# Kernel optimization log

Measured on AMD Instinct MI355X. Metric: run time of the kernel, lower is better.

The kernel has to match this reference:

```python
import jax, jax.numpy as jnp
import numpy as np

H = 8
DK = 32  # head_dim = 256 // 8
SCALE = 1.0 / np.float32(np.sqrt(DK))
EPS = 1e-5


def _ln(x, g, b):
    mu = jnp.mean(x, axis=-1, keepdims=True)
    var = jnp.var(x, axis=-1, keepdims=True)
    return (x - mu) / jnp.sqrt(var + EPS) * g + b


def _lin(x, W, b):
    return x @ W + b


def setup_inputs() -> dict:
    key = jax.random.key(0)
    ks = jax.random.split(key, 16)
    B, M, N, D, F = 4, 64, 512, 256, 1024
    s = 0.02
    inp = {
        "machine_emb": jax.random.normal(ks[0], (B, M, D), jnp.float32),
        "op_emb": jax.random.normal(ks[1], (B, N, D), jnp.float32),
        "edge_emb": jax.random.normal(ks[2], (B, N, M, D), jnp.float32),
        "o2m_mask": jax.random.bernoulli(ks[3], 0.3, (B, N, M)),
    }
    # projection weights stored as (in, out)
    for i, nm in enumerate(["q", "k", "v", "o", "ks", "vs", "e"]):
        inp["W" + nm] = jax.random.normal(ks[4 + i], (D, D), jnp.float32) * s
        inp["b" + nm] = jnp.zeros((D,), jnp.float32)
    # layernorms: norm1 (g1/b1), norm2 (g2/b2), norm_op (gop/bop)
    for nm in ["1", "2", "op"]:
        inp["g" + nm] = jnp.ones((D,), jnp.float32)
        inp["bn" + nm] = jnp.zeros((D,), jnp.float32)
    # FFN
    inp["Wf1"] = jax.random.normal(ks[11], (D, F), jnp.float32) * s
    inp["bf1"] = jnp.zeros((F,), jnp.float32)
    inp["Wf2"] = jax.random.normal(ks[12], (F, D), jnp.float32) * s
    inp["bf2"] = jnp.zeros((D,), jnp.float32)
    return inp


def reference(machine_emb, op_emb, edge_emb, o2m_mask,
              Wq, bq, Wk, bk, Wv, bv, Wo, bo, Wks, bks, Wvs, bvs, We, be,
              g1, bn1, g2, bn2, gop, bnop, Wf1, bf1, Wf2, bf2):
    B, M, D = machine_emb.shape
    N = op_emb.shape[1]

    residual = machine_emb
    machine_norm = _ln(machine_emb, g1, bn1)
    op_norm = _ln(op_emb, gop, bnop)

    # (B, H, M, dk) / (B, H, N, dk)
    q_m = _lin(machine_norm, Wq, bq).reshape(B, M, H, DK).transpose(0, 2, 1, 3)
    k_o = _lin(op_norm, Wk, bk).reshape(B, N, H, DK).transpose(0, 2, 1, 3)
    v_o = _lin(op_norm, Wv, bv).reshape(B, N, H, DK).transpose(0, 2, 1, 3)

    # edge: (B,N,M,D) -> (B,H,M,N,dk)
    edge = _lin(edge_emb, We, be).reshape(B, N, M, H, DK)
    edge = edge.transpose(0, 3, 2, 1, 4)  # bhmnd

    q_total = q_m[:, :, :, None, :] + edge          # (B,H,M,N,dk)
    k_total = k_o[:, :, None, :, :] + edge          # (B,H,M,N,dk)
    v_total = v_o[:, :, None, :, :] + edge          # (B,H,M,N,dk)

    scores = jnp.sum(q_total * k_total, axis=-1) * SCALE  # (B,H,M,N)

    k_self = _lin(machine_norm, Wks, bks).reshape(B, M, H, DK).transpose(0, 2, 1, 3)
    self_scores = jnp.sum(q_m * k_self, axis=-1) * SCALE   # (B,H,M)

    cross_mask = o2m_mask.transpose(0, 2, 1)[:, None, :, :]  # (B,1,M,N)
    combined_scores = jnp.concatenate([self_scores[..., None], scores], axis=-1)  # (B,H,M,1+N)
    self_flag = jnp.ones((B, 1, M, 1), dtype=bool)
    combined_mask = jnp.concatenate([self_flag, jnp.broadcast_to(cross_mask, (B, 1, M, N))], axis=-1)
    combined_scores = jnp.where(combined_mask, combined_scores, -jnp.inf)

    attn = jax.nn.softmax(combined_scores, axis=-1)
    attn = jnp.where(jnp.isnan(attn), 0.0, attn)

    v_self = _lin(machine_norm, Wvs, bvs).reshape(B, M, H, DK).transpose(0, 2, 1, 3)
    combined_values = jnp.concatenate([v_self[:, :, :, None, :], v_total], axis=3)  # (B,H,M,1+N,dk)

    attn_out = jnp.einsum('bhmi,bhmid->bhmd', attn, combined_values)
    attn_out = attn_out.transpose(0, 2, 1, 3).reshape(B, M, D)
    attn_out = _lin(attn_out, Wo, bo)

    machine_emb = residual + attn_out
    h = _ln(machine_emb, g2, bn2)
    ffn = _lin(jax.nn.relu(_lin(h, Wf1, bf1)), Wf2, bf2)
    return machine_emb + ffn
```

## Files before the change

### kernel.cpp

```cpp
#include <hip/hip_runtime.h>
#include <hip/hip_bf16.h>
#include <math.h>

#define H_ 8
#define DK_ 32
#define B_ 4
#define M_ 64
#define N_ 512
#define D_ 256
#define F_ 1024

static constexpr float SCALE = 0.17677669529663687f;
static constexpr float EPS = 1e-5f;

typedef __bf16 bf16x8 __attribute__((ext_vector_type(8)));
typedef float f32x4 __attribute__((ext_vector_type(4)));

__device__ inline float bfbits2f(unsigned int b) {
    union { unsigned int i; float f; } c; c.i = b << 16; return c.f;
}
__device__ inline void unpack8(uint4 u, float* f) {
    f[0] = bfbits2f(u.x & 0xffffu); f[1] = bfbits2f(u.x >> 16);
    f[2] = bfbits2f(u.y & 0xffffu); f[3] = bfbits2f(u.y >> 16);
    f[4] = bfbits2f(u.z & 0xffffu); f[5] = bfbits2f(u.z >> 16);
    f[6] = bfbits2f(u.w & 0xffffu); f[7] = bfbits2f(u.w >> 16);
}

__global__ __launch_bounds__(256) void detect_kernel(const unsigned int* __restrict__ mask,
                                                     int* __restrict__ flags) {
    __shared__ int s2[256];
    int t = threadIdx.x;
    int cgt = 0;
    for (int i = 0; i < 128; ++i) {
        unsigned int w = mask[t * 128 + i];
        if (w > 1u) cgt++;
    }
    s2[t] = cgt;
    __syncthreads();
    if (t == 0) {
        int b = 0;
        for (int i = 0; i < 256; ++i) b += s2[i];
        flags[1] = (b > 0) ? 1 : 0;
    }
}

struct TTArgs {
    const void* src[9];
    void* dst[9];
    int tcum[9];
    int kl[9];
    int nl[9];
};

__global__ __launch_bounds__(256) void prep_transpose(TTArgs a) {
    __shared__ float ld[64][65];
    int bx = blockIdx.x;
    int ti = 0;
    while (bx >= a.tcum[ti]) ti++;
    int j = bx - (ti ? a.tcum[ti - 1] : 0);
    int K = 1 << a.kl[ti], N = 1 << a.nl[ti];
    int ntn = N >> 6;
    int kt = j / ntn, nt = j - kt * ntn;
    const float* src = (const float*)a.src[ti];
    __hip_bfloat16* dst = (__hip_bfloat16*)a.dst[ti];
    int t = threadIdx.x;
    int col = t & 63, r0 = t >> 6;
#pragma unroll
    for (int i = 0; i < 16; ++i) {
        int r = i * 4 + r0;
        ld[r][col] = src[(size_t)(kt * 64 + r) * N + nt * 64 + col];
    }
    __syncthreads();
#pragma unroll
    for (int i = 0; i < 16; ++i) {
        int r = i * 4 + r0;
        dst[(size_t)(nt * 64 + r) * K + kt * 64 + col] = __float2bfloat16(ld[col][r]);
    }
}

__global__ __launch_bounds__(256) void prep_bias(const float* bq, const float* bks,
                                                 const float* bvs, const float* bk,
                                                 const float* bv,
                                                 float* bqksvs, float* bkv) {
    int t = threadIdx.x;
    bqksvs[t] = bq[t];
    bqksvs[256 + t] = bks[t];
    bqksvs[512 + t] = bvs[t];
    bkv[t] = bk[t];
    bkv[256 + t] = bv[t];
}

__device__ inline float block_reduce256(float v, bool is_max, float* sbuf) {
#pragma unroll
    for (int off = 32; off > 0; off >>= 1) {
        float o = __shfl_down(v, off, 64);
        v = is_max ? fmaxf(v, o) : (v + o);
    }
    int lane = threadIdx.x & 63, wid = threadIdx.x >> 6;
    if (lane == 0) sbuf[wid] = v;
    __syncthreads();
    float r;
    if (is_max) r = fmaxf(fmaxf(sbuf[0], sbuf[1]), fmaxf(sbuf[2], sbuf[3]));
    else        r = sbuf[0] + sbuf[1] + sbuf[2] + sbuf[3];
    __syncthreads();
    return r;
}

__global__ __launch_bounds__(256) void ln_kernel(const float* __restrict__ xin,
                                                 const float* __restrict__ g,
                                                 const float* __restrict__ bta,
                                                 __hip_bfloat16* __restrict__ out) {
    __shared__ float sbuf[4];
    int row = blockIdx.x, d = threadIdx.x;
    size_t idx = (size_t)row * 256 + d;
    float x = xin[idx];
    float s  = block_reduce256(x, false, sbuf);
    float ss = block_reduce256(x * x, false, sbuf);
    float mu = s * (1.f / 256.f);
    float var = ss * (1.f / 256.f) - mu * mu;
    float y = (x - mu) * rsqrtf(var + EPS) * g[d] + bta[d];
    out[idx] = __float2bfloat16(y);
}

__global__ __launch_bounds__(256) void gemm64(const __hip_bfloat16* __restrict__ A,
                                              const __hip_bfloat16* __restrict__ BT,
                                              const float* __restrict__ bias,
                                              const float* __restrict__ resid,
                                              void* __restrict__ out,
                                              int K, int ldc, int flags) {
    __shared__ __align__(16) __bf16 As[64 * 40];
    __shared__ __align__(16) __bf16 Bs[64 * 40];
    const int rowBase = blockIdx.x * 64;
    const int colBase = blockIdx.y * 64;
    const int t = threadIdx.x;
    const int w = t >> 6;
    const int l = t & 63;
    const int lrow = l & 15;
    const int lk8 = (l >> 4) * 8;
    const int ar = t >> 2;
    const int ac = (t & 3) * 8;

    f32x4 acc[4] = {};
    for (int k0 = 0; k0 < K; k0 += 32) {
        bf16x8 av = *(const bf16x8*)(A + (size_t)(rowBase + ar) * K + k0 + ac);
        bf16x8 bv = *(const bf16x8*)(BT + (size_t)(colBase + ar) * K + k0 + ac);
        __syncthreads();
        *(bf16x8*)(As + ar * 40 + ac) = av;
        *(bf16x8*)(Bs + ar * 40 + ac) = bv;
        __syncthreads();
        bf16x8 af = *(const bf16x8*)(As + (w * 16 + lrow) * 40 + lk8);
#pragma unroll
        for (int c = 0; c < 4; ++c) {
            bf16x8 bf = *(const bf16x8*)(Bs + (c * 16 + lrow) * 40 + lk8);
            acc[c] = __builtin_amdgcn_mfma_f32_16x16x32_bf16(af, bf, acc[c], 0, 0, 0);
        }
    }
    int rbase = rowBase + w * 16 + ((l >> 4) * 4);
#pragma unroll
    for (int c = 0; c < 4; ++c) {
        int col = colBase + c * 16 + (l & 15);
        float bb = bias[col];
#pragma unroll
        for (int r = 0; r < 4; ++r) {
            int row = rbase + r;
            size_t oi = (size_t)row * ldc + col;
            float v = acc[c][r] + bb;
            if (flags & 1) v = fmaxf(v, 0.f);
            if (flags & 4) v += resid[oi];
            if (flags & 8) ((float*)out)[oi] = v;
            else ((__hip_bfloat16*)out)[oi] = __float2bfloat16(v);
        }
    }
}

__global__ __launch_bounds__(256) void edge_gemm4(const float* __restrict__ E,
                                                  const __hip_bfloat16* __restrict__ WeT,
                                                  const float* __restrict__ be,
                                                  const __hip_bfloat16* __restrict__ qkvs,
                                                  const __hip_bfloat16* __restrict__ kov,
                                                  const void* __restrict__ mask,
                                                  const int* __restrict__ flags,
                                                  __hip_bfloat16* __restrict__ eperm,
                                                  float* __restrict__ scBn) {
    __shared__ __align__(16) __bf16 smem[64 * 272];
    __bf16* As = smem;
    __bf16* Cs = smem;
    const int bn = blockIdx.x;
    const int b = bn >> 9, n = bn & 511;
    const int t = threadIdx.x;
    const int w = t >> 6;
    const int l = t & 63;
    const int lrow = l & 15;
    const int lk8 = (l >> 4) * 8;
    const int ar = t >> 2;
    const int ac = (t & 3) * 8;
    const float* Ab = E + (size_t)bn * 64 * 256;

    f32x4 acc[4][4] = {};
    for (int k0 = 0; k0 < 256; k0 += 32) {
        const float* ap = Ab + (size_t)ar * 256 + k0 + ac;
        float4 x0 = *(const float4*)ap;
        float4 x1 = *(const float4*)(ap + 4);
        bf16x8 av;
        av[0] = (__bf16)x0.x; av[1] = (__bf16)x0.y; av[2] = (__bf16)x0.z; av[3] = (__bf16)x0.w;
        av[4] = (__bf16)x1.x; av[5] = (__bf16)x1.y; av[6] = (__bf16)x1.z; av[7] = (__bf16)x1.w;
        __syncthreads();
        *(bf16x8*)(As + ar * 40 + ac) = av;
        __syncthreads();
        bf16x8 af[4];
#pragma unroll
        for (int rr = 0; rr < 4; ++rr)
            af[rr] = *(const bf16x8*)(As + (rr * 16 + lrow) * 40 + lk8);
#pragma unroll
        for (int c = 0; c < 4; ++c) {
            bf16x8 bf = *(const bf16x8*)(WeT + (size_t)(w * 64 + c * 16 + lrow) * 256 + k0 + lk8);
#pragma unroll
            for (int rr = 0; rr < 4; ++rr)
                acc[rr][c] = __builtin_amdgcn_mfma_f32_16x16x32_bf16(af[rr], bf, acc[rr][c], 0, 0, 0);
        }
    }
    __syncthreads();
#pragma unroll
    for (int c = 0; c < 4; ++c) {
        int col = w * 64 + c * 16 + (l & 15);
        float bb = be[col];
#pragma unroll
        for (int rr = 0; rr < 4; ++rr) {
#pragma unroll
            for (int r = 0; r < 4; ++r) {
                int m = rr * 16 + (l >> 4) * 4 + r;
                Cs[m * 272 + col] = (__bf16)(acc[rr][c][r] + bb);
            }
        }
    }
    __syncthreads();
    const bool u8 = flags[1] != 0;
    const int seg = t & 31;
    const int h = seg >> 2;
    const int dk8 = (seg & 3) * 8;
#pragma unroll
    for (int j = 0; j < 8; ++j) {
        int m = j * 8 + (t >> 5);
        uint4 ev4 = *(const uint4*)(Cs + m * 272 + seg * 8);
        size_t bhm = (size_t)((b * 8 + h) * 64 + m);
        *(uint4*)(eperm + (bhm * 512 + n) * 32 + dk8) = ev4;
        float ev[8], qf[8], kf[8];
        unpack8(ev4, ev);
        uint4 qv4 = *(const uint4*)(qkvs + (size_t)(b * 64 + m) * 768 + h * 32 + dk8);
        uint4 kv4 = *(const uint4*)(kov + (size_t)(b * 512 + n) * 512 + h * 32 + dk8);
        unpack8(qv4, qf);
        unpack8(kv4, kf);
        float p = 0.f;
#pragma unroll
        for (int i = 0; i < 8; ++i)
            p += (qf[i] + ev[i]) * (kf[i] + ev[i]);
        p += __shfl_xor(p, 1, 64);
        p += __shfl_xor(p, 2, 64);
        if ((t & 3) == 0) {
            int mi = (b * 512 + n) * 64 + m;
            int mk = u8 ? (int)((const unsigned char*)mask)[mi] : ((const int*)mask)[mi];
            scBn[(size_t)bn * 512 + h * 64 + m] = mk ? p * SCALE : -__builtin_inff();
        }
    }
}

__global__ __launch_bounds__(256) void transpose_sc(const float* __restrict__ in,
                                                    float* __restrict__ out) {
    __shared__ float ld[64][65];
    int b = blockIdx.z;
    int n0 = blockIdx.x * 64;
    int hm0 = blockIdx.y * 64;
    int t = threadIdx.x;
    int col = t & 63, r0 = t >> 6;
#pragma unroll
    for (int i = 0; i < 16; ++i) {
        int r = i * 4 + r0;
        ld[r][col] = in[((size_t)(b * 512 + n0 + r)) * 512 + hm0 + col];
    }
    __syncthreads();
#pragma unroll
    for (int i = 0; i < 16; ++i) {
        int r = i * 4 + r0;
        out[((size_t)(b * 512 + hm0 + r)) * 512 + n0 + col] = ld[col][r];
    }
}

__global__ __launch_bounds__(256) void smax_attnout(const float* __restrict__ sc,
                                                    const __hip_bfloat16* __restrict__ qkvs,
                                                    const __hip_bfloat16* __restrict__ kov,
                                                    const __hip_bfloat16* __restrict__ eperm,
                                                    __hip_bfloat16* __restrict__ AO) {
    __shared__ float sbuf[4];
    __shared__ float attnS[512];
    __shared__ float selfSc;
    __shared__ float selfA;
    __shared__ float red[16][8];
    int bhm = blockIdx.x;
    int m = bhm & 63;
    int h = (bhm >> 6) & 7;
    int b = bhm >> 9;
    int t = threadIdx.x;
    if (t == 0) {
        const __hip_bfloat16* q  = qkvs + (size_t)(b * 64 + m) * 768 + h * 32;
        const __hip_bfloat16* ks = q + 256;
        float s = 0.f;
        for (int i = 0; i < 32; ++i) s += __bfloat162float(q[i]) * __bfloat162float(ks[i]);
        selfSc = s * SCALE;
    }
    __syncthreads();
    float sv = selfSc;
    float s0 = sc[(size_t)bhm * 512 + t];
    float s1 = sc[(size_t)bhm * 512 + 256 + t];
    float mx = block_reduce256(fmaxf(fmaxf(s0, s1), sv), true, sbuf);
    float e0 = __expf(s0 - mx);
    float e1 = __expf(s1 - mx);
    float eself = __expf(sv - mx);
    float sum = block_reduce256(e0 + e1 + (t == 0 ? eself : 0.f), false, sbuf);
    float inv = 1.f / sum;
    attnS[t] = e0 * inv;
    attnS[256 + t] = e1 * inv;
    if (t == 0) selfA = eself * inv;
    __syncthreads();

    const int d8 = (t & 3) * 8;
    const int ng = t >> 2;
    const int w = t >> 6, l = t & 63;
    const __hip_bfloat16* ebase = eperm + (size_t)bhm * 512 * 32;
    const __hip_bfloat16* vbase = kov + (size_t)(b * 512) * 512 + 256 + h * 32;
    float accv[8] = {};
#pragma unroll
    for (int i = 0; i < 8; ++i) {
        int n = ng + i * 64;
        float a = attnS[n];
        float ev[8], vv[8];
        uint4 e4 = *(const uint4*)(ebase + (size_t)n * 32 + d8);
        uint4 v4 = *(const uint4*)(vbase + (size_t)n * 512 + d8);
        unpack8(e4, ev);
        unpack8(v4, vv);
#pragma unroll
        for (int k = 0; k < 8; ++k) accv[k] += a * (vv[k] + ev[k]);
    }
#pragma unroll
    for (int off = 4; off <= 32; off <<= 1) {
#pragma unroll
        for (int k = 0; k < 8; ++k) accv[k] += __shfl_xor(accv[k], off, 64);
    }
    if ((l >> 2) == 0) {
#pragma unroll
        for (int k = 0; k < 8; ++k) red[w * 4 + (l & 3)][k] = accv[k];
    }
    __syncthreads();
    if (t < 32) {
        int slot = t >> 3, elem = t & 7;
        float r = red[slot][elem] + red[4 + slot][elem] + red[8 + slot][elem] + red[12 + slot][elem];
        float vs = __bfloat162float(qkvs[(size_t)(b * 64 + m) * 768 + 512 + h * 32 + t]);
        r += selfA * vs;
        AO[(size_t)(b * 64 + m) * 256 + h * 32 + t] = __float2bfloat16(r);
    }
}

extern "C" void kernel_launch(void* const* d_in, const int* in_sizes, int n_in,
                              void* d_out, int out_size, void* d_ws, size_t ws_size,
                              hipStream_t stream) {
    const float* machine_emb = (const float*)d_in[0];
    const float* op_emb      = (const float*)d_in[1];
    const float* edge_emb    = (const float*)d_in[2];
    const void*  o2m_mask    = d_in[3];

    char* p = (char*)d_ws;
    int* flags = (int*)p;                        p += 256;
    __hip_bfloat16* WqksvsT = (__hip_bfloat16*)p; p += 196608 * 2;
    __hip_bfloat16* WkvT    = (__hip_bfloat16*)p; p += 131072 * 2;
    __hip_bfloat16* WoT     = (__hip_bfloat16*)p; p += 65536 * 2;
    __hip_bfloat16* WeT     = (__hip_bfloat16*)p; p += 65536 * 2;
    __hip_bfloat16* Wf1T    = (__hip_bfloat16*)p; p += 262144 * 2;
    __hip_bfloat16* Wf2T    = (__hip_bfloat16*)p; p += 262144 * 2;
    float* bqksvs           = (float*)p;          p += 768 * 4;
    float* bkv              = (float*)p;          p += 512 * 4;
    __hip_bfloat16* mnorm   = (__hip_bfloat16*)p; p += 65536 * 2;
    __hip_bfloat16* onorm   = (__hip_bfloat16*)p; p += 524288 * 2;
    __hip_bfloat16* qkvs    = (__hip_bfloat16*)p; p += 196608 * 2;
    __hip_bfloat16* kov     = (__hip_bfloat16*)p; p += 1048576 * 2;
    __hip_bfloat16* eperm   = (__hip_bfloat16*)p; p += (size_t)33554432 * 2;
    float* scBn      = (float*)p;                p += (size_t)1048576 * 4;
    float* scT       = (float*)p;                p += (size_t)1048576 * 4;
    __hip_bfloat16* AO = (__hip_bfloat16*)p;     p += 65536 * 2;
    float* m2        = (float*)p;                p += 65536 * 4;
    __hip_bfloat16* hn = (__hip_bfloat16*)p;     p += 65536 * 2;
    __hip_bfloat16* h1 = (__hip_bfloat16*)p;     p += 262144 * 2;

    TTArgs ta;
    const int srcIdx[9] = {4, 12, 14, 6, 8, 10, 16, 24, 26};
    void* dsts[9] = {WqksvsT, WqksvsT + 65536, WqksvsT + 131072,
                     WkvT, WkvT + 65536, WoT, WeT, Wf1T, Wf2T};
    const int kl9[9] = {8, 8, 8, 8, 8, 8, 8, 8, 10};
    const int nl9[9] = {8, 8, 8, 8, 8, 8, 8, 10, 8};
    int tcum = 0;
    for (int i = 0; i < 9; ++i) {
        ta.src[i] = d_in[srcIdx[i]];
        ta.dst[i] = dsts[i];
        int tiles = (1 << (kl9[i] - 6)) * (1 << (nl9[i] - 6));
        tcum += tiles;
        ta.tcum[i] = tcum;
        ta.kl[i] = kl9[i];
        ta.nl[i] = nl9[i];
    }

    hipLaunchKernelGGL(detect_kernel, dim3(1), dim3(256), 0, stream,
                       (const unsigned int*)o2m_mask, flags);
    hipLaunchKernelGGL(prep_transpose, dim3(tcum), dim3(256), 0, stream, ta);
    hipLaunchKernelGGL(prep_bias, dim3(1), dim3(256), 0, stream,
                       (const float*)d_in[5], (const float*)d_in[13],
                       (const float*)d_in[15], (const float*)d_in[7],
                       (const float*)d_in[9], bqksvs, bkv);

    hipLaunchKernelGGL(ln_kernel, dim3(256), dim3(256), 0, stream,
                       machine_emb, (const float*)d_in[18], (const float*)d_in[19], mnorm);
    hipLaunchKernelGGL(ln_kernel, dim3(2048), dim3(256), 0, stream,
                       op_emb, (const float*)d_in[22], (const float*)d_in[23], onorm);

    hipLaunchKernelGGL(gemm64, dim3(4, 12), dim3(256), 0, stream,
                       mnorm, WqksvsT, bqksvs, nullptr, qkvs, 256, 768, 0);
    hipLaunchKernelGGL(gemm64, dim3(32, 8), dim3(256), 0, stream,
                       onorm, WkvT, bkv, nullptr, kov, 256, 512, 0);

    hipLaunchKernelGGL(edge_gemm4, dim3(2048), dim3(256), 0, stream,
                       edge_emb, WeT, (const float*)d_in[17],
                       qkvs, kov, o2m_mask, flags, eperm, scBn);

    hipLaunchKernelGGL(transpose_sc, dim3(8, 8, 4), dim3(256), 0, stream, scBn, scT);

    hipLaunchKernelGGL(smax_attnout, dim3(2048), dim3(256), 0, stream,
                       scT, qkvs, kov, eperm, AO);

    hipLaunchKernelGGL(gemm64, dim3(4, 4), dim3(256), 0, stream,
                       AO, WoT, (const float*)d_in[11], machine_emb, m2, 256, 256, 4 | 8);
    hipLaunchKernelGGL(ln_kernel, dim3(256), dim3(256), 0, stream,
                       m2, (const float*)d_in[20], (const float*)d_in[21], hn);
    hipLaunchKernelGGL(gemm64, dim3(4, 16), dim3(256), 0, stream,
                       hn, Wf1T, (const float*)d_in[25], nullptr, h1, 256, 1024, 1);
    hipLaunchKernelGGL(gemm64, dim3(4, 4), dim3(256), 0, stream,
                       h1, Wf2T, (const float*)d_in[27], m2, (float*)d_out, 1024, 256, 4 | 8);
}
```

Before: 379.4 us.

## Fuse edge projection, scores, softmax and PV into flash-style kernel with split merge

Replaces the edge GEMM, score transpose and softmax/attention-output kernels with a single flash-attention-style kernel. Each block owns one (b, m) and a quarter of the ops, computes the edge projection with MFMA and applies an online softmax. A small merge kernel then combines the four partial results with the self-attention term. This removes the large materialised bf16 edge tensor (eperm) and the score round-trips through global memory. In exchange the edge reads become strided across n (64*256 floats apart), the k/v loads are scalar, and there are fewer blocks (1024 instead of 2048).

```diff
diff --git a/kernel.cpp b/kernel.cpp
--- a/kernel.cpp
+++ b/kernel.cpp
@@ -18,12 +18,6 @@
 
 __device__ inline float bfbits2f(unsigned int b) {
     union { unsigned int i; float f; } c; c.i = b << 16; return c.f;
-}
-__device__ inline void unpack8(uint4 u, float* f) {
-    f[0] = bfbits2f(u.x & 0xffffu); f[1] = bfbits2f(u.x >> 16);
-    f[2] = bfbits2f(u.y & 0xffffu); f[3] = bfbits2f(u.y >> 16);
-    f[4] = bfbits2f(u.z & 0xffffu); f[5] = bfbits2f(u.z >> 16);
-    f[6] = bfbits2f(u.w & 0xffffu); f[7] = bfbits2f(u.w >> 16);
 }
 
 __global__ __launch_bounds__(256) void detect_kernel(const unsigned int* __restrict__ mask,
@@ -173,190 +167,220 @@
     }
 }
 
-__global__ __launch_bounds__(256) void edge_gemm4(const float* __restrict__ E,
+__global__ __launch_bounds__(256) void edge_flash(const float* __restrict__ E,
                                                   const __hip_bfloat16* __restrict__ WeT,
                                                   const float* __restrict__ be,
                                                   const __hip_bfloat16* __restrict__ qkvs,
                                                   const __hip_bfloat16* __restrict__ kov,
                                                   const void* __restrict__ mask,
                                                   const int* __restrict__ flags,
-                                                  __hip_bfloat16* __restrict__ eperm,
-                                                  float* __restrict__ scBn) {
-    __shared__ __align__(16) __bf16 smem[64 * 272];
-    __bf16* As = smem;
-    __bf16* Cs = smem;
-    const int bn = blockIdx.x;
-    const int b = bn >> 9, n = bn & 511;
+                                                  float* __restrict__ fPV,
+                                                  float* __restrict__ fML) {
+    __shared__ float mbias[128];
+    const int bid = blockIdx.x;
+    const int b  = bid >> 8;
+    const int qq = (bid >> 6) & 3;
+    const int m  = bid & 63;
+    const int n0 = qq * 128;
     const int t = threadIdx.x;
     const int w = t >> 6;
     const int l = t & 63;
-    const int lrow = l & 15;
-    const int lk8 = (l >> 4) * 8;
-    const int ar = t >> 2;
-    const int ac = (t & 3) * 8;
-    const float* Ab = E + (size_t)bn * 64 * 256;
-
-    f32x4 acc[4][4] = {};
-    for (int k0 = 0; k0 < 256; k0 += 32) {
-        const float* ap = Ab + (size_t)ar * 256 + k0 + ac;
-        float4 x0 = *(const float4*)ap;
-        float4 x1 = *(const float4*)(ap + 4);
-        bf16x8 av;
-        av[0] = (__bf16)x0.x; av[1] = (__bf16)x0.y; av[2] = (__bf16)x0.z; av[3] = (__bf16)x0.w;
-        av[4] = (__bf16)x1.x; av[5] = (__bf16)x1.y; av[6] = (__bf16)x1.z; av[7] = (__bf16)x1.w;
-        __syncthreads();
-        *(bf16x8*)(As + ar * 40 + ac) = av;
-        __syncthreads();
-        bf16x8 af[4];
-#pragma unroll
-        for (int rr = 0; rr < 4; ++rr)
-            af[rr] = *(const bf16x8*)(As + (rr * 16 + lrow) * 40 + lk8);
-#pragma unroll
-        for (int c = 0; c < 4; ++c) {
-            bf16x8 bf = *(const bf16x8*)(WeT + (size_t)(w * 64 + c * 16 + lrow) * 256 + k0 + lk8);
+    const int l15 = l & 15;
+    const int lh  = l >> 4;
+
+    if (t < 128) {
+        int n = n0 + t;
+        int mi = (b * 512 + n) * 64 + m;
+        int mk = (flags[1] != 0) ? (int)((const unsigned char*)mask)[mi]
+                                 : ((const int*)mask)[mi];
+        mbias[t] = mk ? 0.f : -1e30f;
+    }
+
+    int   col[4];
+    float qv[4], bev[4];
+#pragma unroll
+    for (int c = 0; c < 4; ++c) {
+        col[c] = w * 64 + c * 16 + l15;
+        qv[c]  = __bfloat162float(qkvs[(size_t)(b * 64 + m) * 768 + col[c]]);
+        bev[c] = be[col[c]];
+    }
+    const __hip_bfloat16* kvb = kov + (size_t)b * 512 * 512;
+    __syncthreads();
+
+    float M[2] = {-1e25f, -1e25f};
+    float L[2] = {0.f, 0.f};
+    float PV[2][2] = {{0.f, 0.f}, {0.f, 0.f}};
+
+    for (int nt = 0; nt < 2; ++nt) {
+        const int ns = n0 + nt * 64;
+        f32x4 acc[4][4] = {};
+        const float* apb = E + ((size_t)((b * 512 + ns + l15) * 64 + m)) * 256 + lh * 8;
+#pragma unroll 2
+        for (int k0 = 0; k0 < 256; k0 += 32) {
+            bf16x8 af[4];
+#pragma unroll
+            for (int rr = 0; rr < 4; ++rr) {
+                const float* ap = apb + (size_t)rr * (16 * 64 * 256) + k0;
+                float4 x0 = *(const float4*)ap;
+                float4 x1 = *(const float4*)(ap + 4);
+                bf16x8 v;
+                v[0] = (__bf16)x0.x; v[1] = (__bf16)x0.y; v[2] = (__bf16)x0.z; v[3] = (__bf16)x0.w;
+                v[4] = (__bf16)x1.x; v[5] = (__bf16)x1.y; v[6] = (__bf16)x1.z; v[7] = (__bf16)x1.w;
+                af[rr] = v;
+            }
+#pragma unroll
+            for (int c = 0; c < 4; ++c) {
+                bf16x8 bv = *(const bf16x8*)(WeT + (size_t)col[c] * 256 + k0 + lh * 8);
+#pragma unroll
+                for (int rr = 0; rr < 4; ++rr)
+                    acc[rr][c] = __builtin_amdgcn_mfma_f32_16x16x32_bf16(af[rr], bv, acc[rr][c], 0, 0, 0);
+            }
+        }
+
+        float s[4][2][4];
+#pragma unroll
+        for (int rr = 0; rr < 4; ++rr) {
+            const int nb = ns + rr * 16 + lh * 4;
+#pragma unroll
+            for (int r = 0; r < 4; ++r) {
+                const size_t krow = (size_t)(nb + r) * 512;
+                float p0 = 0.f, p1 = 0.f;
+#pragma unroll
+                for (int ce = 0; ce < 2; ++ce) {
+                    {
+                        const int c = ce;
+                        float kf = __bfloat162float(kvb[krow + col[c]]);
+                        float ef = acc[rr][c][r] + bev[c];
+                        p0 += (qv[c] + ef) * (kf + ef);
+                    }
+                    {
+                        const int c = 2 + ce;
+                        float kf = __bfloat162float(kvb[krow + col[c]]);
+                        float ef = acc[rr][c][r] + bev[c];
+                        p1 += (qv[c] + ef) * (kf + ef);
+                    }
+                }
+                s[rr][0][r] = p0;
+                s[rr][1][r] = p1;
+            }
+        }
+#pragma unroll
+        for (int rr = 0; rr < 4; ++rr) {
+#pragma unroll
+            for (int r = 0; r < 4; ++r) {
+                float mb = mbias[nt * 64 + rr * 16 + lh * 4 + r];
+#pragma unroll
+                for (int hp = 0; hp < 2; ++hp) {
+                    float v = s[rr][hp][r];
+                    v += __shfl_xor(v, 1);
+                    v += __shfl_xor(v, 2);
+                    v += __shfl_xor(v, 4);
+                    v += __shfl_xor(v, 8);
+                    s[rr][hp][r] = v * SCALE + mb;
+                }
+            }
+        }
+#pragma unroll
+        for (int hp = 0; hp < 2; ++hp) {
+            float tm = s[0][hp][0];
 #pragma unroll
             for (int rr = 0; rr < 4; ++rr)
-                acc[rr][c] = __builtin_amdgcn_mfma_f32_16x16x32_bf16(af[rr], bf, acc[rr][c], 0, 0, 0);
-        }
-    }
-    __syncthreads();
-#pragma unroll
-    for (int c = 0; c < 4; ++c) {
-        int col = w * 64 + c * 16 + (l & 15);
-        float bb = be[col];
+#pragma unroll
+                for (int r = 0; r < 4; ++r) tm = fmaxf(tm, s[rr][hp][r]);
+            tm = fmaxf(tm, __shfl_xor(tm, 16));
+            tm = fmaxf(tm, __shfl_xor(tm, 32));
+            float Mn = fmaxf(M[hp], tm);
+            float f = __expf(M[hp] - Mn);
+            M[hp] = Mn;
+            L[hp] *= f;
+            PV[hp][0] *= f;
+            PV[hp][1] *= f;
+        }
 #pragma unroll
         for (int rr = 0; rr < 4; ++rr) {
-#pragma unroll
-            for (int r = 0; r < 4; ++r) {
-                int m = rr * 16 + (l >> 4) * 4 + r;
-                Cs[m * 272 + col] = (__bf16)(acc[rr][c][r] + bb);
-            }
-        }
-    }
-    __syncthreads();
-    const bool u8 = flags[1] != 0;
-    const int seg = t & 31;
-    const int h = seg >> 2;
-    const int dk8 = (seg & 3) * 8;
-#pragma unroll
-    for (int j = 0; j < 8; ++j) {
-        int m = j * 8 + (t >> 5);
-        uint4 ev4 = *(const uint4*)(Cs + m * 272 + seg * 8);
-        size_t bhm = (size_t)((b * 8 + h) * 64 + m);
-        *(uint4*)(eperm + (bhm * 512 + n) * 32 + dk8) = ev4;
-        float ev[8], qf[8], kf[8];
-        unpack8(ev4, ev);
-        uint4 qv4 = *(const uint4*)(qkvs + (size_t)(b * 64 + m) * 768 + h * 32 + dk8);
-        uint4 kv4 = *(const uint4*)(kov + (size_t)(b * 512 + n) * 512 + h * 32 + dk8);
-        unpack8(qv4, qf);
-        unpack8(kv4, kf);
-        float p = 0.f;
-#pragma unroll
-        for (int i = 0; i < 8; ++i)
-            p += (qf[i] + ev[i]) * (kf[i] + ev[i]);
-        p += __shfl_xor(p, 1, 64);
-        p += __shfl_xor(p, 2, 64);
-        if ((t & 3) == 0) {
-            int mi = (b * 512 + n) * 64 + m;
-            int mk = u8 ? (int)((const unsigned char*)mask)[mi] : ((const int*)mask)[mi];
-            scBn[(size_t)bn * 512 + h * 64 + m] = mk ? p * SCALE : -__builtin_inff();
-        }
-    }
-}
-
-__global__ __launch_bounds__(256) void transpose_sc(const float* __restrict__ in,
-                                                    float* __restrict__ out) {
-    __shared__ float ld[64][65];
-    int b = blockIdx.z;
-    int n0 = blockIdx.x * 64;
-    int hm0 = blockIdx.y * 64;
-    int t = threadIdx.x;
-    int col = t & 63, r0 = t >> 6;
-#pragma unroll
-    for (int i = 0; i < 16; ++i) {
-        int r = i * 4 + r0;
-        ld[r][col] = in[((size_t)(b * 512 + n0 + r)) * 512 + hm0 + col];
-    }
-    __syncthreads();
-#pragma unroll
-    for (int i = 0; i < 16; ++i) {
-        int r = i * 4 + r0;
-        out[((size_t)(b * 512 + hm0 + r)) * 512 + n0 + col] = ld[col][r];
-    }
-}
-
-__global__ __launch_bounds__(256) void smax_attnout(const float* __restrict__ sc,
-                                                    const __hip_bfloat16* __restrict__ qkvs,
-                                                    const __hip_bfloat16* __restrict__ kov,
-                                                    const __hip_bfloat16* __restrict__ eperm,
-                                                    __hip_bfloat16* __restrict__ AO) {
-    __shared__ float sbuf[4];
-    __shared__ float attnS[512];
-    __shared__ float selfSc;
-    __shared__ float selfA;
-    __shared__ float red[16][8];
-    int bhm = blockIdx.x;
-    int m = bhm & 63;
-    int h = (bhm >> 6) & 7;
-    int b = bhm >> 9;
-    int t = threadIdx.x;
-    if (t == 0) {
-        const __hip_bfloat16* q  = qkvs + (size_t)(b * 64 + m) * 768 + h * 32;
-        const __hip_bfloat16* ks = q + 256;
-        float s = 0.f;
-        for (int i = 0; i < 32; ++i) s += __bfloat162float(q[i]) * __bfloat162float(ks[i]);
-        selfSc = s * SCALE;
-    }
-    __syncthreads();
-    float sv = selfSc;
-    float s0 = sc[(size_t)bhm * 512 + t];
-    float s1 = sc[(size_t)bhm * 512 + 256 + t];
-    float mx = block_reduce256(fmaxf(fmaxf(s0, s1), sv), true, sbuf);
-    float e0 = __expf(s0 - mx);
-    float e1 = __expf(s1 - mx);
-    float eself = __expf(sv - mx);
-    float sum = block_reduce256(e0 + e1 + (t == 0 ? eself : 0.f), false, sbuf);
-    float inv = 1.f / sum;
-    attnS[t] = e0 * inv;
-    attnS[256 + t] = e1 * inv;
-    if (t == 0) selfA = eself * inv;
-    __syncthreads();
-
-    const int d8 = (t & 3) * 8;
-    const int ng = t >> 2;
-    const int w = t >> 6, l = t & 63;
-    const __hip_bfloat16* ebase = eperm + (size_t)bhm * 512 * 32;
-    const __hip_bfloat16* vbase = kov + (size_t)(b * 512) * 512 + 256 + h * 32;
-    float accv[8] = {};
-#pragma unroll
-    for (int i = 0; i < 8; ++i) {
-        int n = ng + i * 64;
-        float a = attnS[n];
-        float ev[8], vv[8];
-        uint4 e4 = *(const uint4*)(ebase + (size_t)n * 32 + d8);
-        uint4 v4 = *(const uint4*)(vbase + (size_t)n * 512 + d8);
-        unpack8(e4, ev);
-        unpack8(v4, vv);
-#pragma unroll
-        for (int k = 0; k < 8; ++k) accv[k] += a * (vv[k] + ev[k]);
-    }
-#pragma unroll
-    for (int off = 4; off <= 32; off <<= 1) {
-#pragma unroll
-        for (int k = 0; k < 8; ++k) accv[k] += __shfl_xor(accv[k], off, 64);
-    }
-    if ((l >> 2) == 0) {
-#pragma unroll
-        for (int k = 0; k < 8; ++k) red[w * 4 + (l & 3)][k] = accv[k];
-    }
-    __syncthreads();
-    if (t < 32) {
-        int slot = t >> 3, elem = t & 7;
-        float r = red[slot][elem] + red[4 + slot][elem] + red[8 + slot][elem] + red[12 + slot][elem];
-        float vs = __bfloat162float(qkvs[(size_t)(b * 64 + m) * 768 + 512 + h * 32 + t]);
-        r += selfA * vs;
-        AO[(size_t)(b * 64 + m) * 256 + h * 32 + t] = __float2bfloat16(r);
-    }
+            const int nb = ns + rr * 16 + lh * 4;
+#pragma unroll
+            for (int hp = 0; hp < 2; ++hp) {
+#pragma unroll
+                for (int r = 0; r < 4; ++r) {
+                    const size_t vrow = (size_t)(nb + r) * 512 + 256;
+                    float a = __expf(s[rr][hp][r] - M[hp]);
+                    L[hp] += a;
+                    float ef0 = acc[rr][2 * hp][r]     + bev[2 * hp];
+                    float ef1 = acc[rr][2 * hp + 1][r] + bev[2 * hp + 1];
+                    float vf0 = __bfloat162float(kvb[vrow + col[2 * hp]]);
+                    float vf1 = __bfloat162float(kvb[vrow + col[2 * hp + 1]]);
+                    PV[hp][0] += a * (ef0 + vf0);
+                    PV[hp][1] += a * (ef1 + vf1);
+                }
+            }
+        }
+    }
+
+#pragma unroll
+    for (int hp = 0; hp < 2; ++hp) {
+        L[hp] += __shfl_xor(L[hp], 16);
+        L[hp] += __shfl_xor(L[hp], 32);
+#pragma unroll
+        for (int ce = 0; ce < 2; ++ce) {
+            PV[hp][ce] += __shfl_xor(PV[hp][ce], 16);
+            PV[hp][ce] += __shfl_xor(PV[hp][ce], 32);
+        }
+    }
+    const int part = (b * 64 + m) * 4 + qq;
+    if (lh == 0) {
+#pragma unroll
+        for (int hp = 0; hp < 2; ++hp) {
+            int h = 2 * w + hp;
+#pragma unroll
+            for (int ce = 0; ce < 2; ++ce)
+                fPV[((size_t)part * 8 + h) * 32 + ce * 16 + l15] = PV[hp][ce];
+            if (l15 == 0) {
+                fML[((size_t)part * 8 + h) * 2 + 0] = M[hp];
+                fML[((size_t)part * 8 + h) * 2 + 1] = L[hp];
+            }
+        }
+    }
+}
+
+__global__ __launch_bounds__(256) void flash_merge(const float* __restrict__ fPV,
+                                                   const float* __restrict__ fML,
+                                                   const __hip_bfloat16* __restrict__ qkvs,
+                                                   __hip_bfloat16* __restrict__ AO) {
+    const int bm = blockIdx.x;
+    const int t = threadIdx.x;
+    const int h = t >> 5, dk = t & 31;
+    const int col = h * 32 + dk;
+    const __hip_bfloat16* qb = qkvs + (size_t)bm * 768;
+    float qf  = __bfloat162float(qb[col]);
+    float ksf = __bfloat162float(qb[256 + col]);
+    float p = qf * ksf;
+    p += __shfl_xor(p, 1);
+    p += __shfl_xor(p, 2);
+    p += __shfl_xor(p, 4);
+    p += __shfl_xor(p, 8);
+    p += __shfl_xor(p, 16);
+    float sself = p * SCALE;
+    float Mst = sself;
+    float Mq[4], Lq[4], Pq[4];
+    const int part0 = bm * 4;
+#pragma unroll
+    for (int q = 0; q < 4; ++q) {
+        Mq[q] = fML[((size_t)(part0 + q) * 8 + h) * 2 + 0];
+        Lq[q] = fML[((size_t)(part0 + q) * 8 + h) * 2 + 1];
+        Pq[q] = fPV[((size_t)(part0 + q) * 8 + h) * 32 + dk];
+        Mst = fmaxf(Mst, Mq[q]);
+    }
+    float fs = __expf(sself - Mst);
+    float Ltot = fs;
+    float Ptot = fs * __bfloat162float(qb[512 + col]);
+#pragma unroll
+    for (int q = 0; q < 4; ++q) {
+        float fq = __expf(Mq[q] - Mst);
+        Ltot += Lq[q] * fq;
+        Ptot += Pq[q] * fq;
+    }
+    AO[(size_t)bm * 256 + col] = __float2bfloat16(Ptot / Ltot);
 }
 
 extern "C" void kernel_launch(void* const* d_in, const int* in_sizes, int n_in,
@@ -381,9 +405,8 @@
     __hip_bfloat16* onorm   = (__hip_bfloat16*)p; p += 524288 * 2;
     __hip_bfloat16* qkvs    = (__hip_bfloat16*)p; p += 196608 * 2;
     __hip_bfloat16* kov     = (__hip_bfloat16*)p; p += 1048576 * 2;
-    __hip_bfloat16* eperm   = (__hip_bfloat16*)p; p += (size_t)33554432 * 2;
-    float* scBn      = (float*)p;                p += (size_t)1048576 * 4;
-    float* scT       = (float*)p;                p += (size_t)1048576 * 4;
+    float* fPV              = (float*)p;          p += 262144 * 4;
+    float* fML              = (float*)p;          p += 16384 * 4;
     __hip_bfloat16* AO = (__hip_bfloat16*)p;     p += 65536 * 2;
     float* m2        = (float*)p;                p += 65536 * 4;
     __hip_bfloat16* hn = (__hip_bfloat16*)p;     p += 65536 * 2;
@@ -424,14 +447,12 @@
     hipLaunchKernelGGL(gemm64, dim3(32, 8), dim3(256), 0, stream,
                        onorm, WkvT, bkv, nullptr, kov, 256, 512, 0);
 
-    hipLaunchKernelGGL(edge_gemm4, dim3(2048), dim3(256), 0, stream,
+    hipLaunchKernelGGL(edge_flash, dim3(1024), dim3(256), 0, stream,
                        edge_emb, WeT, (const float*)d_in[17],
-                       qkvs, kov, o2m_mask, flags, eperm, scBn);
-
-    hipLaunchKernelGGL(transpose_sc, dim3(8, 8, 4), dim3(256), 0, stream, scBn, scT);
-
-    hipLaunchKernelGGL(smax_attnout, dim3(2048), dim3(256), 0, stream,
-                       scT, qkvs, kov, eperm, AO);
+                       qkvs, kov, o2m_mask, flags, fPV, fML);
+
+    hipLaunchKernelGGL(flash_merge, dim3(256), dim3(256), 0, stream,
+                       fPV, fML, qkvs, AO);
 
     hipLaunchKernelGGL(gemm64, dim3(4, 4), dim3(256), 0, stream,
                        AO, WoT, (const float*)d_in[11], machine_emb, m2, 256, 256, 4 | 8);
```

Result: slower. 404.7 us (+6.7%).

## Merge prep, layernorm, QKV GEMM launches and write scores pre-transposed

Applied to the files above, without the earlier changes.

Folds bias packing and flag reset into the weight-transpose kernel, and merges both input layernorms with a parallel mask-width detection that uses atomicOr. The two projection GEMMs are combined into one dual-problem launch. The edge GEMM now writes scores directly in (b,h,m,n) order, which removes the separate transpose kernel and its scratch buffer. This cuts several launches and a 4 MB round trip, at the cost of scattered 4-byte score stores from the edge kernel and an ordering dependency between the flag reset and the atomic detection.

```diff
diff --git a/kernel.cpp b/kernel.cpp
--- a/kernel.cpp
+++ b/kernel.cpp
@@ -26,35 +26,29 @@
     f[6] = bfbits2f(u.w & 0xffffu); f[7] = bfbits2f(u.w >> 16);
 }
 
-__global__ __launch_bounds__(256) void detect_kernel(const unsigned int* __restrict__ mask,
-                                                     int* __restrict__ flags) {
-    __shared__ int s2[256];
-    int t = threadIdx.x;
-    int cgt = 0;
-    for (int i = 0; i < 128; ++i) {
-        unsigned int w = mask[t * 128 + i];
-        if (w > 1u) cgt++;
-    }
-    s2[t] = cgt;
-    __syncthreads();
-    if (t == 0) {
-        int b = 0;
-        for (int i = 0; i < 256; ++i) b += s2[i];
-        flags[1] = (b > 0) ? 1 : 0;
-    }
-}
-
 struct TTArgs {
     const void* src[9];
     void* dst[9];
     int tcum[9];
     int kl[9];
     int nl[9];
+    const float* bq; const float* bks; const float* bvs; const float* bk; const float* bv;
+    float* bqksvs; float* bkv; int* flags;
 };
 
-__global__ __launch_bounds__(256) void prep_transpose(TTArgs a) {
+__global__ __launch_bounds__(256) void prep_all(TTArgs a) {
     __shared__ float ld[64][65];
     int bx = blockIdx.x;
+    int t = threadIdx.x;
+    if (bx >= a.tcum[8]) {
+        a.bqksvs[t] = a.bq[t];
+        a.bqksvs[256 + t] = a.bks[t];
+        a.bqksvs[512 + t] = a.bvs[t];
+        a.bkv[t] = a.bk[t];
+        a.bkv[256 + t] = a.bv[t];
+        if (t == 0) a.flags[1] = 0;
+        return;
+    }
     int ti = 0;
     while (bx >= a.tcum[ti]) ti++;
     int j = bx - (ti ? a.tcum[ti - 1] : 0);
@@ -63,7 +57,6 @@
     int kt = j / ntn, nt = j - kt * ntn;
     const float* src = (const float*)a.src[ti];
     __hip_bfloat16* dst = (__hip_bfloat16*)a.dst[ti];
-    int t = threadIdx.x;
     int col = t & 63, r0 = t >> 6;
 #pragma unroll
     for (int i = 0; i < 16; ++i) {
@@ -78,18 +71,6 @@
     }
 }
 
-__global__ __launch_bounds__(256) void prep_bias(const float* bq, const float* bks,
-                                                 const float* bvs, const float* bk,
-                                                 const float* bv,
-                                                 float* bqksvs, float* bkv) {
-    int t = threadIdx.x;
-    bqksvs[t] = bq[t];
-    bqksvs[256 + t] = bks[t];
-    bqksvs[512 + t] = bvs[t];
-    bkv[t] = bk[t];
-    bkv[256 + t] = bv[t];
-}
-
 __device__ inline float block_reduce256(float v, bool is_max, float* sbuf) {
 #pragma unroll
     for (int off = 32; off > 0; off >>= 1) {
@@ -104,6 +85,36 @@
     else        r = sbuf[0] + sbuf[1] + sbuf[2] + sbuf[3];
     __syncthreads();
     return r;
+}
+
+__global__ __launch_bounds__(256) void ln_detect(const float* __restrict__ me,
+                                                 const float* __restrict__ oe,
+                                                 const float* __restrict__ g1v,
+                                                 const float* __restrict__ b1v,
+                                                 const float* __restrict__ gov,
+                                                 const float* __restrict__ bov,
+                                                 __hip_bfloat16* __restrict__ mnorm,
+                                                 __hip_bfloat16* __restrict__ onorm,
+                                                 const unsigned int* __restrict__ mask,
+                                                 int* __restrict__ flags) {
+    __shared__ float sbuf[4];
+    int bx = blockIdx.x, t = threadIdx.x;
+    if (bx >= 2304) {
+        uint4 v = ((const uint4*)mask)[(size_t)(bx - 2304) * 256 + t];
+        if (v.x > 1u || v.y > 1u || v.z > 1u || v.w > 1u) atomicOr(flags + 1, 1);
+        return;
+    }
+    const float* xin; const float* g; const float* bta; __hip_bfloat16* out; int row;
+    if (bx < 256) { xin = me; g = g1v; bta = b1v; out = mnorm; row = bx; }
+    else          { xin = oe; g = gov; bta = bov; out = onorm; row = bx - 256; }
+    size_t idx = (size_t)row * 256 + t;
+    float x = xin[idx];
+    float s  = block_reduce256(x, false, sbuf);
+    float ss = block_reduce256(x * x, false, sbuf);
+    float mu = s * (1.f / 256.f);
+    float var = ss * (1.f / 256.f) - mu * mu;
+    float y = (x - mu) * rsqrtf(var + EPS) * g[t] + bta[t];
+    out[idx] = __float2bfloat16(y);
 }
 
 __global__ __launch_bounds__(256) void ln_kernel(const float* __restrict__ xin,
@@ -173,6 +184,59 @@
     }
 }
 
+__global__ __launch_bounds__(256) void gemm64_dual(const __hip_bfloat16* __restrict__ A0,
+                                                   const __hip_bfloat16* __restrict__ BT0,
+                                                   const float* __restrict__ bias0,
+                                                   __hip_bfloat16* __restrict__ out0,
+                                                   const __hip_bfloat16* __restrict__ A1,
+                                                   const __hip_bfloat16* __restrict__ BT1,
+                                                   const float* __restrict__ bias1,
+                                                   __hip_bfloat16* __restrict__ out1) {
+    __shared__ __align__(16) __bf16 As[64 * 40];
+    __shared__ __align__(16) __bf16 Bs[64 * 40];
+    const int id = blockIdx.x;
+    const __hip_bfloat16* A; const __hip_bfloat16* BT; const float* bias;
+    __hip_bfloat16* out; int bx, by, ldc;
+    if (id < 48) { A = A0; BT = BT0; bias = bias0; out = out0; bx = id & 3;  by = id >> 2; ldc = 768; }
+    else { int j = id - 48; A = A1; BT = BT1; bias = bias1; out = out1; bx = j & 31; by = j >> 5; ldc = 512; }
+    const int rowBase = bx * 64;
+    const int colBase = by * 64;
+    const int t = threadIdx.x;
+    const int w = t >> 6;
+    const int l = t & 63;
+    const int lrow = l & 15;
+    const int lk8 = (l >> 4) * 8;
+    const int ar = t >> 2;
+    const int ac = (t & 3) * 8;
+
+    f32x4 acc[4] = {};
+    for (int k0 = 0; k0 < 256; k0 += 32) {
+        bf16x8 av = *(const bf16x8*)(A + (size_t)(rowBase + ar) * 256 + k0 + ac);
+        bf16x8 bv = *(const bf16x8*)(BT + (size_t)(colBase + ar) * 256 + k0 + ac);
+        __syncthreads();
+        *(bf16x8*)(As + ar * 40 + ac) = av;
+        *(bf16x8*)(Bs + ar * 40 + ac) = bv;
+        __syncthreads();
+        bf16x8 af = *(const bf16x8*)(As + (w * 16 + lrow) * 40 + lk8);
+#pragma unroll
+        for (int c = 0; c < 4; ++c) {
+            bf16x8 bf = *(const bf16x8*)(Bs + (c * 16 + lrow) * 40 + lk8);
+            acc[c] = __builtin_amdgcn_mfma_f32_16x16x32_bf16(af, bf, acc[c], 0, 0, 0);
+        }
+    }
+    int rbase = rowBase + w * 16 + ((l >> 4) * 4);
+#pragma unroll
+    for (int c = 0; c < 4; ++c) {
+        int col = colBase + c * 16 + (l & 15);
+        float bb = bias[col];
+#pragma unroll
+        for (int r = 0; r < 4; ++r) {
+            int row = rbase + r;
+            out[(size_t)row * ldc + col] = __float2bfloat16(acc[c][r] + bb);
+        }
+    }
+}
+
 __global__ __launch_bounds__(256) void edge_gemm4(const float* __restrict__ E,
                                                   const __hip_bfloat16* __restrict__ WeT,
                                                   const float* __restrict__ be,
@@ -181,7 +245,7 @@
                                                   const void* __restrict__ mask,
                                                   const int* __restrict__ flags,
                                                   __hip_bfloat16* __restrict__ eperm,
-                                                  float* __restrict__ scBn) {
+                                                  float* __restrict__ scT) {
     __shared__ __align__(16) __bf16 smem[64 * 272];
     __bf16* As = smem;
     __bf16* Cs = smem;
@@ -259,29 +323,8 @@
         if ((t & 3) == 0) {
             int mi = (b * 512 + n) * 64 + m;
             int mk = u8 ? (int)((const unsigned char*)mask)[mi] : ((const int*)mask)[mi];
-            scBn[(size_t)bn * 512 + h * 64 + m] = mk ? p * SCALE : -__builtin_inff();
-        }
-    }
-}
-
-__global__ __launch_bounds__(256) void transpose_sc(const float* __restrict__ in,
-                                                    float* __restrict__ out) {
-    __shared__ float ld[64][65];
-    int b = blockIdx.z;
-    int n0 = blockIdx.x * 64;
-    int hm0 = blockIdx.y * 64;
-    int t = threadIdx.x;
-    int col = t & 63, r0 = t >> 6;
-#pragma unroll
-    for (int i = 0; i < 16; ++i) {
-        int r = i * 4 + r0;
-        ld[r][col] = in[((size_t)(b * 512 + n0 + r)) * 512 + hm0 + col];
-    }
-    __syncthreads();
-#pragma unroll
-    for (int i = 0; i < 16; ++i) {
-        int r = i * 4 + r0;
-        out[((size_t)(b * 512 + hm0 + r)) * 512 + n0 + col] = ld[col][r];
+            scT[(bhm << 9) + n] = mk ? p * SCALE : -__builtin_inff();
+        }
     }
 }
 
@@ -382,7 +425,6 @@
     __hip_bfloat16* qkvs    = (__hip_bfloat16*)p; p += 196608 * 2;
     __hip_bfloat16* kov     = (__hip_bfloat16*)p; p += 1048576 * 2;
     __hip_bfloat16* eperm   = (__hip_bfloat16*)p; p += (size_t)33554432 * 2;
-    float* scBn      = (float*)p;                p += (size_t)1048576 * 4;
     float* scT       = (float*)p;                p += (size_t)1048576 * 4;
     __hip_bfloat16* AO = (__hip_bfloat16*)p;     p += 65536 * 2;
     float* m2        = (float*)p;                p += 65536 * 4;
@@ -405,30 +447,26 @@
         ta.kl[i] = kl9[i];
         ta.nl[i] = nl9[i];
     }
-
-    hipLaunchKernelGGL(detect_kernel, dim3(1), dim3(256), 0, stream,
-                       (const unsigned int*)o2m_mask, flags);
-    hipLaunchKernelGGL(prep_transpose, dim3(tcum), dim3(256), 0, stream, ta);
-    hipLaunchKernelGGL(prep_bias, dim3(1), dim3(256), 0, stream,
-                       (const float*)d_in[5], (const float*)d_in[13],
-                       (const float*)d_in[15], (const float*)d_in[7],
-                       (const float*)d_in[9], bqksvs, bkv);
-
-    hipLaunchKernelGGL(ln_kernel, dim3(256), dim3(256), 0, stream,
-                       machine_emb, (const float*)d_in[18], (const float*)d_in[19], mnorm);
-    hipLaunchKernelGGL(ln_kernel, dim3(2048), dim3(256), 0, stream,
-                       op_emb, (const float*)d_in[22], (const float*)d_in[23], onorm);
-
-    hipLaunchKernelGGL(gemm64, dim3(4, 12), dim3(256), 0, stream,
-                       mnorm, WqksvsT, bqksvs, nullptr, qkvs, 256, 768, 0);
-    hipLaunchKernelGGL(gemm64, dim3(32, 8), dim3(256), 0, stream,
-                       onorm, WkvT, bkv, nullptr, kov, 256, 512, 0);
+    ta.bq = (const float*)d_in[5];  ta.bks = (const float*)d_in[13];
+    ta.bvs = (const float*)d_in[15]; ta.bk = (const float*)d_in[7];
+    ta.bv = (const float*)d_in[9];
+    ta.bqksvs = bqksvs; ta.bkv = bkv; ta.flags = flags;
+
+    hipLaunchKernelGGL(prep_all, dim3(tcum + 1), dim3(256), 0, stream, ta);
+
+    hipLaunchKernelGGL(ln_detect, dim3(2336), dim3(256), 0, stream,
+                       machine_emb, op_emb,
+                       (const float*)d_in[18], (const float*)d_in[19],
+                       (const float*)d_in[22], (const float*)d_in[23],
+                       mnorm, onorm, (const unsigned int*)o2m_mask, flags);
+
+    hipLaunchKernelGGL(gemm64_dual, dim3(304), dim3(256), 0, stream,
+                       mnorm, WqksvsT, bqksvs, qkvs,
+                       onorm, WkvT, bkv, kov);
 
     hipLaunchKernelGGL(edge_gemm4, dim3(2048), dim3(256), 0, stream,
                        edge_emb, WeT, (const float*)d_in[17],
-                       qkvs, kov, o2m_mask, flags, eperm, scBn);
-
-    hipLaunchKernelGGL(transpose_sc, dim3(8, 8, 4), dim3(256), 0, stream, scBn, scT);
+                       qkvs, kov, o2m_mask, flags, eperm, scT);
 
     hipLaunchKernelGGL(smax_attnout, dim3(2048), dim3(256), 0, stream,
                        scT, qkvs, kov, eperm, AO);
```

Result: faster. 356.2 us (-6.1%).
